# Performance work log

Hardware: AMD Instinct MI355X
Metric: run time of the kernel (lower is better)

## Reference

```python
import jax, jax.numpy as jnp
import numpy as np

DN = ('NCHW', 'OIHW', 'NCHW')

def conv(x, w, b=None, stride=(1, 1), pad=((0, 0), (0, 0))):
    y = jax.lax.conv_general_dilated(x, w, stride, pad, dimension_numbers=DN)
    return y if b is None else y + b[None, :, None, None]

def conv_t(x, w, b, stride, pad):
    # PyTorch ConvTranspose2d: weight (in, out, kH, kW), output (H-1)*s - 2p + k
    kH, kW = w.shape[2], w.shape[3]
    wt = jnp.flip(w, axis=(2, 3)).swapaxes(0, 1)  # -> (out, in, kH, kW)
    y = jax.lax.conv_general_dilated(
        x, wt, (1, 1),
        ((kH - 1 - pad[0], kH - 1 - pad[0]), (kW - 1 - pad[1], kW - 1 - pad[1])),
        lhs_dilation=stride, dimension_numbers=DN)
    return y + b[None, :, None, None]

def res_stack(x, rw1, rw2):
    # Residual: x + conv1x1(relu(conv3x3(relu(x)))), then final relu
    for i in range(rw1.shape[0]):
        h = conv(jax.nn.relu(x), rw1[i], None, (1, 1), ((1, 1), (1, 1)))
        h = conv(jax.nn.relu(h), rw2[i], None, (1, 1), ((0, 0), (0, 0)))
        x = x + h
    return jax.nn.relu(x)

def setup_inputs() -> dict:
    key = jax.random.key(0)
    ks = jax.random.split(key, 24)
    def w(i, shape, s=0.05):
        return jax.random.normal(ks[i], shape, jnp.float32) * s
    K, D = 512, 64
    inp = {
        'x': jax.random.normal(ks[0], (32, 2, 400, 600), jnp.float32),
        'enc_w1': w(1, (64, 2, 10, 11)), 'enc_b1': w(2, (64,)),
        'enc_w2': w(3, (128, 64, 12, 12), 0.02), 'enc_b2': w(4, (128,)),
        'enc_w3': w(5, (128, 128, 3, 3)), 'enc_b3': w(6, (128,)),
        'enc_res_w1': w(7, (2, 64, 128, 3, 3)), 'enc_res_w2': w(8, (2, 128, 64, 1, 1)),
        'pre_w': w(9, (64, 128, 1, 1)), 'pre_b': w(10, (64,)),
        'emb': jax.random.uniform(ks[11], (K, D), jnp.float32, -1.0 / K, 1.0 / K),
        'dec_w1': w(12, (128, 64, 3, 3)), 'dec_b1': w(13, (128,)),
        'dec_res_w1': w(14, (2, 64, 128, 3, 3)), 'dec_res_w2': w(15, (2, 128, 64, 1, 1)),
        'dec_tw1': w(16, (128, 64, 12, 12), 0.02), 'dec_tb1': w(17, (64,)),
        'dec_tw2': w(18, (64, 2, 10, 11)), 'dec_tb2': w(19, (2,)),
        'reset': 0,
    }
    return inp

def reference(x, enc_w1, enc_b1, enc_w2, enc_b2, enc_w3, enc_b3, enc_res_w1,
              enc_res_w2, pre_w, pre_b, emb, dec_w1, dec_b1, dec_res_w1,
              dec_res_w2, dec_tw1, dec_tb1, dec_tw2, dec_tb2, reset):
    commitment_cost = 0.25
    K = emb.shape[0]
    # Encoder
    h = jax.nn.relu(conv(x, enc_w1, enc_b1, (8, 9), ((1, 1), (1, 1))))
    h = jax.nn.relu(conv(h, enc_w2, enc_b2, (10, 10), ((1, 1), (1, 1))))
    h = conv(h, enc_w3, enc_b3, (1, 1), ((1, 1), (1, 1)))
    h = res_stack(h, enc_res_w1, enc_res_w2)
    z = conv(h, pre_w, pre_b)  # [B, D, H, W]
    # VectorQuantizer (eval mode)
    zin = z.transpose(0, 2, 3, 1)  # [B, H, W, D]
    B, H, W, D = zin.shape
    flat = zin.reshape(-1, D)
    dist = (jnp.sum(flat ** 2, axis=1, keepdims=True)
            + jnp.sum(emb ** 2, axis=1)
            - 2.0 * flat @ emb.T)  # [N, K]
    idx = jnp.argmin(dist, axis=1)  # [N]
    q = emb[idx].reshape(B, H, W, D)
    e_latent = jnp.mean((jax.lax.stop_gradient(q) - zin) ** 2)
    q_latent = jnp.mean((q - jax.lax.stop_gradient(zin)) ** 2)
    loss = q_latent + commitment_cost * e_latent
    q_st = zin + jax.lax.stop_gradient(q - zin)  # straight-through
    counts = jnp.zeros((K,), jnp.float32).at[idx].add(1.0)
    avg_probs = counts / flat.shape[0]
    perplexity = jnp.exp(-jnp.sum(avg_probs * jnp.log(avg_probs + 1e-10)))
    q_nchw = q_st.transpose(0, 3, 1, 2)
    # Decoder
    d = conv(q_nchw, dec_w1, dec_b1, (1, 1), ((1, 1), (1, 1)))
    d = res_stack(d, dec_res_w1, dec_res_w2)
    d = jax.nn.relu(conv_t(d, dec_tw1, dec_tb1, (10, 10), (1, 1)))
    recon = conv_t(d, dec_tw2, dec_tb2, (8, 9), (1, 1))
    return loss, recon, perplexity
```

## Files before the change

kernel.cpp:

```cpp
#include <hip/hip_runtime.h>
#include <math.h>


__global__ __launch_bounds__(256) void conv1_k(const float* __restrict__ x,
                                               const float* __restrict__ w,
                                               const float* __restrict__ b,
                                               float* __restrict__ y)
{
    __shared__ float xs[2 * 10 * 596];
    const int blk = blockIdx.x;
    const int n = blk / 50, oh = blk % 50;
    const int tid = threadIdx.x;
    const int ih0 = oh * 8 - 1;
    for (int i = tid; i < 2 * 10 * 596; i += 256) {
        int c = i / 5960, rem = i % 5960;
        int r = rem / 596, j = rem % 596;
        int ih = ih0 + r, iw = j - 1;
        float v = 0.f;
        if (ih >= 0 && ih < 400 && iw >= 0 && iw < 600)
            v = x[((n * 2 + c) * 400 + ih) * 600 + iw];
        xs[i] = v;
    }
    __syncthreads();
    for (int i = tid; i < 32 * 66; i += 256) {
        int oc = i / 66, ow = i % 66;
        int col = ow * 9;
        float a0 = 0.f, a1 = 0.f;
        for (int c = 0; c < 2; ++c) {
            const float* wp0 = w + ((oc)      * 2 + c) * 110;
            const float* wp1 = w + ((oc + 32) * 2 + c) * 110;
            const float* xp  = xs + c * 5960 + col;
            for (int kh = 0; kh < 10; ++kh) {
                #pragma unroll
                for (int kw = 0; kw < 11; ++kw) {
                    float xv = xp[kh * 596 + kw];
                    a0 += xv * wp0[kh * 11 + kw];
                    a1 += xv * wp1[kh * 11 + kw];
                }
            }
        }
        y[((n * 64 + oc)      * 50 + oh) * 66 + ow] = fmaxf(a0 + b[oc], 0.f);
        y[((n * 64 + oc + 32) * 50 + oh) * 66 + ow] = fmaxf(a1 + b[oc + 32], 0.f);
    }
}

__global__ __launch_bounds__(256) void repack_oihw_k(const float* __restrict__ w,
                                                     float* __restrict__ wt,
                                                     int OC, int IC, int KH, int KW)
{
    int i = blockIdx.x * 256 + threadIdx.x;
    int total = OC * IC * KH * KW;
    if (i >= total) return;
    int oc = i % OC; int t = i / OC;
    int kw = t % KW; int kh = (t / KW) % KH; int c = t / (KW * KH);
    wt[i] = w[((oc * IC + c) * KH + kh) * KW + kw];
}

__global__ __launch_bounds__(256) void repack_iohw_k(const float* __restrict__ w,
                                                     float* __restrict__ wt,
                                                     int IC, int OC, int KH, int KW)
{
    int i = blockIdx.x * 256 + threadIdx.x;
    int total = OC * IC * KH * KW;
    if (i >= total) return;
    int oc = i % OC; int t = i / OC;
    int kw = t % KW; int kh = (t / KW) % KH; int c = t / (KW * KH);
    wt[i] = w[((c * OC + oc) * KH + kh) * KW + kw];
}

__device__ __forceinline__ float fetch_oihw(const float* __restrict__ w, int j,
                                            int OC, int IC, int KH, int KW)
{
    int oc = j % OC; int t = j / OC;
    int kw = t % KW; int kh = (t / KW) % KH; int c = t / (KW * KH);
    return w[((oc * IC + c) * KH + kh) * KW + kw];
}

__global__ __launch_bounds__(256) void repack_small_k(
    const float* __restrict__ enc_w3, const float* __restrict__ er1,
    const float* __restrict__ er2, const float* __restrict__ pre_w,
    const float* __restrict__ dec_w1, const float* __restrict__ dr1,
    const float* __restrict__ dr2, float* __restrict__ dst)
{
    int i = blockIdx.x * 256 + threadIdx.x;
    if (i >= 557056) return;
    float v;
    if (i < 147456)       v = fetch_oihw(enc_w3,        i,          128, 128, 3, 3);
    else if (i < 221184)  v = fetch_oihw(er1,           i - 147456,  64, 128, 3, 3);
    else if (i < 294912)  v = fetch_oihw(er1 + 73728,   i - 221184,  64, 128, 3, 3);
    else if (i < 303104)  v = fetch_oihw(er2,           i - 294912, 128,  64, 1, 1);
    else if (i < 311296)  v = fetch_oihw(er2 + 8192,    i - 303104, 128,  64, 1, 1);
    else if (i < 319488)  v = fetch_oihw(pre_w,         i - 311296,  64, 128, 1, 1);
    else if (i < 393216)  v = fetch_oihw(dec_w1,        i - 319488, 128,  64, 3, 3);
    else if (i < 466944)  v = fetch_oihw(dr1,           i - 393216,  64, 128, 3, 3);
    else if (i < 540672)  v = fetch_oihw(dr1 + 73728,   i - 466944,  64, 128, 3, 3);
    else if (i < 548864)  v = fetch_oihw(dr2,           i - 540672, 128,  64, 1, 1);
    else                  v = fetch_oihw(dr2 + 8192,    i - 548864, 128,  64, 1, 1);
    dst[i] = v;
}

__global__ __launch_bounds__(512) void conv2_k2(const float* __restrict__ x,
                                                const float* __restrict__ wt,
                                                const float* __restrict__ b,
                                                float* __restrict__ y)
{
    __shared__ float xs[16 * 12 * 64];
    __shared__ float sred[4 * 128 * 6];
    const int tid = threadIdx.x;
    const int oc = tid & 127, sub = tid >> 7;
    const int n = blockIdx.x / 5, oh = blockIdx.x % 5;
    const int ih0 = oh * 10 - 1;
    float acc[6] = {0, 0, 0, 0, 0, 0};
    for (int cc = 0; cc < 4; ++cc) {
        __syncthreads();
        for (int i = tid; i < 12288; i += 512) {
            int col = i & 63; int t2 = i >> 6;
            int r = t2 % 12; int c = t2 / 12;
            int ih = ih0 + r, iw = col - 1;
            float v = 0.f;
            if (ih >= 0 && ih < 50 && iw >= 0 && iw < 66)
                v = x[((n * 64 + cc * 16 + c) * 50 + ih) * 66 + iw];
            xs[i] = v;
        }
        __syncthreads();
        for (int c = 0; c < 16; ++c) {
            for (int kh = sub * 3; kh < sub * 3 + 3; ++kh) {
                float xr[64];
                #pragma unroll
                for (int k = 0; k < 16; ++k)
                    *(float4*)&xr[4 * k] = *(const float4*)&xs[(c * 12 + kh) * 64 + 4 * k];
                const float* wp = wt + ((cc * 16 + c) * 144 + kh * 12) * 128 + oc;
                #pragma unroll
                for (int kw = 0; kw < 12; ++kw) {
                    float wv = wp[kw * 128];
                    #pragma unroll
                    for (int ow = 0; ow < 6; ++ow)
                        acc[ow] += xr[ow * 10 + kw] * wv;
                }
            }
        }
    }
    for (int j = 0; j < 6; ++j) sred[(sub * 128 + oc) * 6 + j] = acc[j];
    __syncthreads();
    if (sub == 0) {
        float bias = b[oc];
        #pragma unroll
        for (int j = 0; j < 6; ++j) {
            float v = acc[j] + sred[(128 + oc) * 6 + j] + sred[(256 + oc) * 6 + j]
                    + sred[(384 + oc) * 6 + j] + bias;
            y[((n * 128 + oc) * 5 + oh) * 6 + j] = fmaxf(v, 0.f);
        }
    }
}


template<int CIN, int COUT, bool RELU_IN>
__device__ __forceinline__ void conv3x3_stage(const float* __restrict__ src,
                                              const float* __restrict__ wg,
                                              const float* __restrict__ bias,
                                              float* __restrict__ dst,
                                              float* __restrict__ WS, int tid)
{
    constexpr int G  = 1024 / COUT;
    constexpr int NP = (30 + G - 1) / G;
    const int oc = tid % COUT;
    const int g  = tid / COUT;
    const int px0 = (30 * g) / G;
    const int np  = (30 * (g + 1)) / G - px0;
    float acc[NP];
    float bv = bias ? bias[oc] : 0.f;
    #pragma unroll
    for (int j = 0; j < NP; ++j) acc[j] = bv;
    for (int cc0 = 0; cc0 < CIN; cc0 += 16) {
        __syncthreads();
        const float* wsrc = wg + cc0 * 9 * COUT;
        for (int i = tid; i < 16 * 9 * COUT; i += 1024) WS[i] = wsrc[i];
        __syncthreads();
        for (int c = 0; c < 16; ++c) {
            const float* sc = src + (cc0 + c) * 30;
            const float* wc = WS + c * 9 * COUT + oc;
            #pragma unroll
            for (int kh = 0; kh < 3; ++kh) {
                #pragma unroll
                for (int kw = 0; kw < 3; ++kw) {
                    float wv = wc[(kh * 3 + kw) * COUT];
                    #pragma unroll
                    for (int j = 0; j < NP; ++j) {
                        if (j < np) {
                            int px = px0 + j;
                            int oh = px / 6, ow = px - oh * 6;
                            int ih = oh + kh - 1, iw = ow + kw - 1;
                            if ((unsigned)ih < 5u && (unsigned)iw < 6u) {
                                float xv = sc[ih * 6 + iw];
                                if (RELU_IN) xv = fmaxf(xv, 0.f);
                                acc[j] += xv * wv;
                            }
                        }
                    }
                }
            }
        }
    }
    #pragma unroll
    for (int j = 0; j < NP; ++j)
        if (j < np) dst[oc * 30 + px0 + j] = acc[j];
}

template<int CIN, int COUT, bool RELU_IN, bool ACCUM>
__device__ __forceinline__ void conv1x1_stage(const float* __restrict__ src,
                                              const float* __restrict__ wg,
                                              const float* __restrict__ bias,
                                              float* __restrict__ dst,
                                              float* __restrict__ WS, int tid)
{
    constexpr int G  = 1024 / COUT;
    constexpr int NP = (30 + G - 1) / G;
    const int oc = tid % COUT;
    const int g  = tid / COUT;
    const int px0 = (30 * g) / G;
    const int np  = (30 * (g + 1)) / G - px0;
    __syncthreads();
    for (int i = tid; i < CIN * COUT; i += 1024) WS[i] = wg[i];
    __syncthreads();
    float acc[NP];
    float bv = bias ? bias[oc] : 0.f;
    #pragma unroll
    for (int j = 0; j < NP; ++j) acc[j] = bv;
    for (int c = 0; c < CIN; ++c) {
        float wv = WS[c * COUT + oc];
        #pragma unroll
        for (int j = 0; j < NP; ++j) {
            if (j < np) {
                float xv = src[c * 30 + px0 + j];
                if (RELU_IN) xv = fmaxf(xv, 0.f);
                acc[j] += xv * wv;
            }
        }
    }
    #pragma unroll
    for (int j = 0; j < NP; ++j) {
        if (j < np) {
            if (ACCUM) dst[oc * 30 + px0 + j] += acc[j];
            else       dst[oc * 30 + px0 + j] = acc[j];
        }
    }
}

__global__ __launch_bounds__(1024) void chain_k(
    const float* __restrict__ h2, const float* __restrict__ wsm,
    const float* __restrict__ enc_b3, const float* __restrict__ pre_b,
    const float* __restrict__ emb, const float* __restrict__ dec_b1,
    float* __restrict__ xpad, float* __restrict__ counts,
    float* __restrict__ loss_sum)
{
    __shared__ float A[3840], B[3840], T[1920], Z[1920];
    __shared__ float WS[16 * 9 * 128];
    const int n = blockIdx.x;
    const int tid = threadIdx.x;
    for (int i = tid; i < 3840; i += 1024) A[i] = h2[n * 3840 + i];
    conv3x3_stage<128, 128, false>(A, wsm, enc_b3, B, WS, tid);
    conv3x3_stage<128, 64, true>(B, wsm + 147456, nullptr, T, WS, tid);
    conv1x1_stage<64, 128, true, true>(T, wsm + 294912, nullptr, B, WS, tid);
    conv3x3_stage<128, 64, true>(B, wsm + 221184, nullptr, T, WS, tid);
    conv1x1_stage<64, 128, true, true>(T, wsm + 303104, nullptr, B, WS, tid);
    conv1x1_stage<128, 64, true, false>(B, wsm + 311296, pre_b, Z, WS, tid);
    __syncthreads();
    const int lane = tid & 63, wid = tid >> 6;
    for (int px = wid; px < 30; px += 16) {
        float zr[64];
        #pragma unroll
        for (int d = 0; d < 64; ++d) zr[d] = Z[d * 30 + px];
        float best = 1e30f; int bestk = 0;
        for (int jk = 0; jk < 8; ++jk) {
            int k = lane + jk * 64;
            const float* ep = emb + k * 64;
            float dist = 0.f;
            #pragma unroll 8
            for (int d = 0; d < 64; ++d) { float df = ep[d] - zr[d]; dist += df * df; }
            if (dist < best) { best = dist; bestk = k; }
        }
        for (int off = 32; off; off >>= 1) {
            float ob = __shfl_down(best, off); int ok = __shfl_down(bestk, off);
            if (ob < best || (ob == best && ok < bestk)) { best = ob; bestk = ok; }
        }
        bestk = __shfl(bestk, 0);
        float ev = emb[bestk * 64 + lane];
        T[lane * 30 + px] = ev;
        float df = ev - Z[lane * 30 + px]; df *= df;
        for (int off = 32; off; off >>= 1) df += __shfl_down(df, off);
        if (lane == 0) { atomicAdd(loss_sum, df); atomicAdd(&counts[bestk], 1.f); }
    }
    __syncthreads();
    conv3x3_stage<64, 128, false>(T, wsm + 319488, dec_b1, A, WS, tid);
    conv3x3_stage<128, 64, true>(A, wsm + 393216, nullptr, T, WS, tid);
    conv1x1_stage<64, 128, true, true>(T, wsm + 540672, nullptr, A, WS, tid);
    conv3x3_stage<128, 64, true>(A, wsm + 466944, nullptr, T, WS, tid);
    conv1x1_stage<64, 128, true, true>(T, wsm + 548864, nullptr, A, WS, tid);
    __syncthreads();
    for (int i = tid; i < 7168; i += 1024) {
        int col = i & 7, r = (i >> 3) % 7, c = i / 56;
        float v = 0.f;
        if (r >= 1 && r <= 5 && col >= 1 && col <= 6)
            v = fmaxf(A[c * 30 + (r - 1) * 6 + col - 1], 0.f);
        xpad[n * 7168 + i] = v;
    }
}


template<bool TR, bool TS>
__device__ __forceinline__ void ct1_accum(const float* __restrict__ xs0,
                                          const float* __restrict__ xs1,
                                          const float* __restrict__ wt,
                                          int R, int S, int m0, int lane,
                                          float acc[6])
{
    #pragma unroll 2
    for (int c = 0; c < 128; ++c) {
        float x1[7], x0[7];
        #pragma unroll
        for (int k = 0; k < 7; ++k) x1[k] = xs1[c * 8 + m0 + k];
        if (TR) {
            #pragma unroll
            for (int k = 0; k < 7; ++k) x0[k] = xs0[c * 8 + m0 + k];
        }
        float wA = wt[(c * 144 + R * 12 + S) * 64 + lane];
        #pragma unroll
        for (int j = 0; j < 6; ++j) acc[j] += x1[j + 1] * wA;
        if (TS) {
            float wB = wt[(c * 144 + R * 12 + S + 10) * 64 + lane];
            #pragma unroll
            for (int j = 0; j < 6; ++j) acc[j] += x1[j] * wB;
        }
        if (TR) {
            float wC = wt[(c * 144 + (R + 10) * 12 + S) * 64 + lane];
            #pragma unroll
            for (int j = 0; j < 6; ++j) acc[j] += x0[j + 1] * wC;
            if (TS) {
                float wD = wt[(c * 144 + (R + 10) * 12 + S + 10) * 64 + lane];
                #pragma unroll
                for (int j = 0; j < 6; ++j) acc[j] += x0[j] * wD;
            }
        }
    }
}

__global__ __launch_bounds__(256) void convt1_k3(const float* __restrict__ xp,
                                                 const float* __restrict__ wt,
                                                 const float* __restrict__ b,
                                                 float* __restrict__ y)
{
    __shared__ float xs[2][128][8];
    const int bi = blockIdx.x;
    const int n = bi / 50, oh = bi % 50;
    const int q = (oh + 1) / 10, R = (oh + 1) % 10;
    const int tid = threadIdx.x;
    for (int i = tid; i < 2048; i += 256) {
        int col = i & 7, c = (i >> 3) & 127, r = i >> 10;
        ((float*)xs)[i] = xp[((n * 128 + c) * 7 + q + r) * 8 + col];
    }
    __syncthreads();
    const int lane = tid & 63, wv = tid >> 6;
    const float bias = b[lane];
    const float* xs0 = &xs[0][0][0];
    const float* xs1 = &xs[1][0][0];
    for (int si = 0; si < 3; ++si) {
        int S = wv + si * 4;
        if (S >= 10) break;
        int m0 = (S == 0) ? 1 : 0;
        float acc[6] = {0, 0, 0, 0, 0, 0};
        if (R < 2) {
            if (S < 2) ct1_accum<true, true>(xs0, xs1, wt, R, S, m0, lane, acc);
            else       ct1_accum<true, false>(xs0, xs1, wt, R, S, m0, lane, acc);
        } else {
            if (S < 2) ct1_accum<false, true>(xs0, xs1, wt, R, S, m0, lane, acc);
            else       ct1_accum<false, false>(xs0, xs1, wt, R, S, m0, lane, acc);
        }
        float* yp = y + ((n * 64 + lane) * 52 + oh + 1) * 62 + 10 * m0 + S;
        #pragma unroll
        for (int j = 0; j < 6; ++j) yp[10 * j] = fmaxf(acc[j] + bias, 0.f);
    }
}


template<bool TR, bool TS>
__device__ __forceinline__ void ct2_accum(const float* __restrict__ xs0,
                                          const float* __restrict__ xs1,
                                          const float* __restrict__ wt2,
                                          int R, int S, int m,
                                          float& a0, float& a1)
{
    #pragma unroll 4
    for (int c = 0; c < 64; ++c) {
        float x1a = xs1[c * 64 + m + 1];
        float2 wA = *(const float2*)&wt2[(c * 110 + R * 11 + S) * 2];
        a0 += x1a * wA.x; a1 += x1a * wA.y;
        if (TS) {
            float x1b = xs1[c * 64 + m];
            float2 wB = *(const float2*)&wt2[(c * 110 + R * 11 + S + 9) * 2];
            a0 += x1b * wB.x; a1 += x1b * wB.y;
        }
        if (TR) {
            float x0a = xs0[c * 64 + m + 1];
            float2 wC = *(const float2*)&wt2[(c * 110 + (R + 8) * 11 + S) * 2];
            a0 += x0a * wC.x; a1 += x0a * wC.y;
            if (TS) {
                float x0b = xs0[c * 64 + m];
                float2 wD = *(const float2*)&wt2[(c * 110 + (R + 8) * 11 + S + 9) * 2];
                a0 += x0b * wD.x; a1 += x0b * wD.y;
            }
        }
    }
}

__global__ __launch_bounds__(256) void convt2_k3(const float* __restrict__ xd,
                                                 const float* __restrict__ wt2,
                                                 const float* __restrict__ bb,
                                                 float* __restrict__ out)
{
    __shared__ float xs[2][64][64];
    const int bi = blockIdx.x;
    const int n = bi / 51, io = bi % 51;
    const int tid = threadIdx.x;
    for (int i = tid; i < 2 * 64 * 64; i += 256) {
        int col = i & 63, c = (i >> 6) & 63, r = i >> 12;
        float v = 0.f;
        if (col < 62) v = xd[((n * 64 + c) * 52 + io + r) * 62 + col];
        ((float*)xs)[i] = v;
    }
    __syncthreads();
    const float b0 = bb[0], b1 = bb[1];
    const int lane = tid & 63, wv = tid >> 6;
    if (lane < 60) {
        const float* xs0 = &xs[0][0][0];
        const float* xs1 = &xs[1][0][0];
        for (int pp = 0; pp < 18; ++pp) {
            int p = wv * 18 + pp;
            int R = p / 9, S = p % 9;
            int oh = 8 * io + R - 1;
            if (oh < 0 || oh >= 400) continue;
            int m = lane + ((S == 0) ? 1 : 0);
            float a0 = 0.f, a1 = 0.f;
            if (R < 2) {
                if (S < 2) ct2_accum<true, true>(xs0, xs1, wt2, R, S, m, a0, a1);
                else       ct2_accum<true, false>(xs0, xs1, wt2, R, S, m, a0, a1);
            } else {
                if (S < 2) ct2_accum<false, true>(xs0, xs1, wt2, R, S, m, a0, a1);
                else       ct2_accum<false, false>(xs0, xs1, wt2, R, S, m, a0, a1);
            }
            int ow = 9 * m + S - 1;
            float* yp = out + ((size_t)(n * 2) * 400 + oh) * 540 + ow;
            yp[0] = a0 + b0;
            yp[400 * 540] = a1 + b1;
        }
    }
}

__global__ __launch_bounds__(512) void fin_k(const float* __restrict__ counts,
                                             const float* __restrict__ loss_sum,
                                             float* __restrict__ out, int out_size)
{
    __shared__ float red[512];
    int t = threadIdx.x;
    float c = counts[t];
    float p = c * (1.0f / 960.0f);
    red[t] = p * logf(p + 1e-10f);
    __syncthreads();
    for (int s = 256; s > 0; s >>= 1) {
        if (t < s) red[t] += red[t + s];
        __syncthreads();
    }
    if (t == 0) {
        out[out_size - 1] = expf(-red[0]);
        out[0] = loss_sum[0] * 1.25f / 61440.0f;
    }
}

extern "C" void kernel_launch(void* const* d_in, const int* in_sizes, int n_in,
                              void* d_out, int out_size, void* d_ws, size_t ws_size,
                              hipStream_t stream)
{
    const float* x          = (const float*)d_in[0];
    const float* enc_w1     = (const float*)d_in[1];
    const float* enc_b1     = (const float*)d_in[2];
    const float* enc_w2     = (const float*)d_in[3];
    const float* enc_b2     = (const float*)d_in[4];
    const float* enc_w3     = (const float*)d_in[5];
    const float* enc_b3     = (const float*)d_in[6];
    const float* enc_res_w1 = (const float*)d_in[7];
    const float* enc_res_w2 = (const float*)d_in[8];
    const float* pre_w      = (const float*)d_in[9];
    const float* pre_b      = (const float*)d_in[10];
    const float* emb        = (const float*)d_in[11];
    const float* dec_w1     = (const float*)d_in[12];
    const float* dec_b1     = (const float*)d_in[13];
    const float* dec_res_w1 = (const float*)d_in[14];
    const float* dec_res_w2 = (const float*)d_in[15];
    const float* dec_tw1    = (const float*)d_in[16];
    const float* dec_tb1    = (const float*)d_in[17];
    const float* dec_tw2    = (const float*)d_in[18];
    const float* dec_tb2    = (const float*)d_in[19];

    float* ws  = (float*)d_ws;
    float* out = (float*)d_out;

    float* h1       = ws;
    float* dmid     = ws;
    float* h2       = ws + 6758400;
    float* counts   = ws + 6881280;
    float* loss_sum = ws + 6881792;
    float* wtA      = ws + 6881856;
    float* wt2      = ws + 8061504;
    float* xpad     = ws + 8075584;
    float* wsm      = ws + 8304960;

    hipMemsetAsync(counts, 0, 513 * sizeof(float), stream);

    repack_oihw_k<<<4608, 256, 0, stream>>>(enc_w2, wtA, 128, 64, 12, 12);
    conv1_k<<<1600, 256, 0, stream>>>(x, enc_w1, enc_b1, h1);
    conv2_k2<<<160, 512, 0, stream>>>(h1, wtA, enc_b2, h2);

    repack_small_k<<<2176, 256, 0, stream>>>(enc_w3, enc_res_w1, enc_res_w2, pre_w,
                                             dec_w1, dec_res_w1, dec_res_w2, wsm);
    chain_k<<<32, 1024, 0, stream>>>(h2, wsm, enc_b3, pre_b, emb, dec_b1,
                                     xpad, counts, loss_sum);

    repack_iohw_k<<<4608, 256, 0, stream>>>(dec_tw1, wtA, 128, 64, 12, 12);
    repack_iohw_k<<<55, 256, 0, stream>>>(dec_tw2, wt2, 64, 2, 10, 11);
    hipMemsetAsync(dmid, 0, (size_t)6602752 * sizeof(float), stream);
    convt1_k3<<<1600, 256, 0, stream>>>(xpad, wtA, dec_tb1, dmid);
    convt2_k3<<<1632, 256, 0, stream>>>(dmid, wt2, dec_tb2, out + 1);

    fin_k<<<1, 512, 0, stream>>>(counts, loss_sum, out, out_size);
}
```

Before: 2.249 ms.

## Split input channels across wave groups in chain kernel convs with shared-memory reduction

Rewrites the fused mid-network conv stages so each 64-thread group handles a slice of input channels for all 30 pixels, reading weights straight from global memory into registers. Partial sums are combined through two shared buffers with shared-memory atomics. This removes the staged weight copies into shared memory and the per-pixel bounds and index arithmetic. In exchange it needs large register arrays (up to 60 accumulators plus weights) at 1024 threads per block and adds atomic reduction traffic.

Result: faster. 2.177 ms (-3.2%).

```diff
diff --git a/kernel.cpp b/kernel.cpp
--- a/kernel.cpp
+++ b/kernel.cpp
@@ -154,96 +154,104 @@
 }
 
 
-template<int CIN, int COUT, bool RELU_IN>
-__device__ __forceinline__ void conv3x3_stage(const float* __restrict__ src,
-                                              const float* __restrict__ wg,
-                                              const float* __restrict__ bias,
-                                              float* __restrict__ dst,
-                                              float* __restrict__ WS, int tid)
-{
-    constexpr int G  = 1024 / COUT;
-    constexpr int NP = (30 + G - 1) / G;
-    const int oc = tid % COUT;
-    const int g  = tid / COUT;
-    const int px0 = (30 * g) / G;
-    const int np  = (30 * (g + 1)) / G - px0;
-    float acc[NP];
-    float bv = bias ? bias[oc] : 0.f;
+template<int CIN, int COUT, int KS, bool RELU_IN, bool ACCUM, bool HASBIAS>
+__device__ __forceinline__ void stagef(const float* __restrict__ src,
+                                       const float* __restrict__ wg,
+                                       const float* __restrict__ bias,
+                                       float* __restrict__ dst,
+                                       float* __restrict__ P,
+                                       float* __restrict__ Q,
+                                       int slot, int g)
+{
+    constexpr int OCPT = COUT / 64;
+    constexpr int CPT  = CIN / 16;
+    constexpr int NV   = 30 * OCPT;
+    constexpr int STR  = NV + 1;
+    float acc[OCPT][30];
     #pragma unroll
-    for (int j = 0; j < NP; ++j) acc[j] = bv;
-    for (int cc0 = 0; cc0 < CIN; cc0 += 16) {
-        __syncthreads();
-        const float* wsrc = wg + cc0 * 9 * COUT;
-        for (int i = tid; i < 16 * 9 * COUT; i += 1024) WS[i] = wsrc[i];
-        __syncthreads();
-        for (int c = 0; c < 16; ++c) {
-            const float* sc = src + (cc0 + c) * 30;
-            const float* wc = WS + c * 9 * COUT + oc;
-            #pragma unroll
-            for (int kh = 0; kh < 3; ++kh) {
-                #pragma unroll
-                for (int kw = 0; kw < 3; ++kw) {
-                    float wv = wc[(kh * 3 + kw) * COUT];
+    for (int o = 0; o < OCPT; ++o)
+        #pragma unroll
+        for (int j = 0; j < 30; ++j) acc[o][j] = 0.f;
+
+    const int c0 = g * CPT;
+    for (int cc = 0; cc < CPT; ++cc) {
+        const int c = c0 + cc;
+        const float* sc = src + c * 30;
+        if (KS == 3) {
+            const float* wp = wg + c * 9 * COUT + slot;
+            float w[OCPT][9];
+            #pragma unroll
+            for (int t = 0; t < 9; ++t)
+                #pragma unroll
+                for (int o = 0; o < OCPT; ++o) w[o][t] = wp[t * COUT + o * 64];
+            #pragma unroll
+            for (int rho = 0; rho < 5; ++rho) {
+                float xr[6];
+                #pragma unroll
+                for (int q2 = 0; q2 < 6; ++q2) {
+                    float xv = sc[rho * 6 + q2];
+                    xr[q2] = RELU_IN ? fmaxf(xv, 0.f) : xv;
+                }
+                #pragma unroll
+                for (int kh = 0; kh < 3; ++kh) {
+                    const int r = rho + 1 - kh;
+                    if (r < 0 || r > 4) continue;
                     #pragma unroll
-                    for (int j = 0; j < NP; ++j) {
-                        if (j < np) {
-                            int px = px0 + j;
-                            int oh = px / 6, ow = px - oh * 6;
-                            int ih = oh + kh - 1, iw = ow + kw - 1;
-                            if ((unsigned)ih < 5u && (unsigned)iw < 6u) {
-                                float xv = sc[ih * 6 + iw];
-                                if (RELU_IN) xv = fmaxf(xv, 0.f);
-                                acc[j] += xv * wv;
-                            }
+                    for (int kw = 0; kw < 3; ++kw) {
+                        #pragma unroll
+                        for (int pc = 0; pc < 6; ++pc) {
+                            const int gam = pc + kw - 1;
+                            if (gam < 0 || gam > 5) continue;
+                            #pragma unroll
+                            for (int o = 0; o < OCPT; ++o)
+                                acc[o][r * 6 + pc] += xr[gam] * w[o][kh * 3 + kw];
                         }
                     }
                 }
             }
-        }
-    }
-    #pragma unroll
-    for (int j = 0; j < NP; ++j)
-        if (j < np) dst[oc * 30 + px0 + j] = acc[j];
-}
-
-template<int CIN, int COUT, bool RELU_IN, bool ACCUM>
-__device__ __forceinline__ void conv1x1_stage(const float* __restrict__ src,
-                                              const float* __restrict__ wg,
-                                              const float* __restrict__ bias,
-                                              float* __restrict__ dst,
-                                              float* __restrict__ WS, int tid)
-{
-    constexpr int G  = 1024 / COUT;
-    constexpr int NP = (30 + G - 1) / G;
-    const int oc = tid % COUT;
-    const int g  = tid / COUT;
-    const int px0 = (30 * g) / G;
-    const int np  = (30 * (g + 1)) / G - px0;
-    __syncthreads();
-    for (int i = tid; i < CIN * COUT; i += 1024) WS[i] = wg[i];
-    __syncthreads();
-    float acc[NP];
-    float bv = bias ? bias[oc] : 0.f;
-    #pragma unroll
-    for (int j = 0; j < NP; ++j) acc[j] = bv;
-    for (int c = 0; c < CIN; ++c) {
-        float wv = WS[c * COUT + oc];
-        #pragma unroll
-        for (int j = 0; j < NP; ++j) {
-            if (j < np) {
-                float xv = src[c * 30 + px0 + j];
+        } else {
+            float w[OCPT];
+            #pragma unroll
+            for (int o = 0; o < OCPT; ++o) w[o] = wg[c * COUT + slot + o * 64];
+            #pragma unroll
+            for (int j = 0; j < 30; ++j) {
+                float xv = sc[j];
                 if (RELU_IN) xv = fmaxf(xv, 0.f);
-                acc[j] += xv * wv;
-            }
-        }
-    }
-    #pragma unroll
-    for (int j = 0; j < NP; ++j) {
-        if (j < np) {
-            if (ACCUM) dst[oc * 30 + px0 + j] += acc[j];
-            else       dst[oc * 30 + px0 + j] = acc[j];
-        }
-    }
+                #pragma unroll
+                for (int o = 0; o < OCPT; ++o) acc[o][j] += xv * w[o];
+            }
+        }
+    }
+    float* buf = (g < 8) ? Q : P;
+    if (g == 0 || g == 8) {
+        #pragma unroll
+        for (int o = 0; o < OCPT; ++o)
+            #pragma unroll
+            for (int j = 0; j < 30; ++j) buf[slot * STR + o * 30 + j] = acc[o][j];
+    }
+    __syncthreads();
+    if (g != 0 && g != 8) {
+        #pragma unroll
+        for (int o = 0; o < OCPT; ++o)
+            #pragma unroll
+            for (int j = 0; j < 30; ++j)
+                atomicAdd(&buf[slot * STR + o * 30 + j], acc[o][j]);
+    }
+    __syncthreads();
+    if (g == 0) {
+        #pragma unroll
+        for (int o = 0; o < OCPT; ++o) {
+            const int oc = slot + o * 64;
+            float bv = HASBIAS ? bias[oc] : 0.f;
+            #pragma unroll
+            for (int j = 0; j < 30; ++j) {
+                float v = Q[slot * STR + o * 30 + j] + P[slot * STR + o * 30 + j] + bv;
+                if (ACCUM) dst[oc * 30 + j] += v;
+                else       dst[oc * 30 + j] = v;
+            }
+        }
+    }
+    __syncthreads();
 }
 
 __global__ __launch_bounds__(1024) void chain_k(
@@ -254,25 +262,25 @@
     float* __restrict__ loss_sum)
 {
     __shared__ float A[3840], B[3840], T[1920], Z[1920];
-    __shared__ float WS[16 * 9 * 128];
+    __shared__ float P[64 * 61], Q[64 * 61];
     const int n = blockIdx.x;
     const int tid = threadIdx.x;
+    const int slot = tid & 63, g = tid >> 6;
     for (int i = tid; i < 3840; i += 1024) A[i] = h2[n * 3840 + i];
-    conv3x3_stage<128, 128, false>(A, wsm, enc_b3, B, WS, tid);
-    conv3x3_stage<128, 64, true>(B, wsm + 147456, nullptr, T, WS, tid);
-    conv1x1_stage<64, 128, true, true>(T, wsm + 294912, nullptr, B, WS, tid);
-    conv3x3_stage<128, 64, true>(B, wsm + 221184, nullptr, T, WS, tid);
-    conv1x1_stage<64, 128, true, true>(T, wsm + 303104, nullptr, B, WS, tid);
-    conv1x1_stage<128, 64, true, false>(B, wsm + 311296, pre_b, Z, WS, tid);
-    __syncthreads();
-    const int lane = tid & 63, wid = tid >> 6;
-    for (int px = wid; px < 30; px += 16) {
+    __syncthreads();
+    stagef<128, 128, 3, false, false, true>(A, wsm, enc_b3, B, P, Q, slot, g);
+    stagef<128, 64, 3, true, false, false>(B, wsm + 147456, nullptr, T, P, Q, slot, g);
+    stagef<64, 128, 1, true, true, false>(T, wsm + 294912, nullptr, B, P, Q, slot, g);
+    stagef<128, 64, 3, true, false, false>(B, wsm + 221184, nullptr, T, P, Q, slot, g);
+    stagef<64, 128, 1, true, true, false>(T, wsm + 303104, nullptr, B, P, Q, slot, g);
+    stagef<128, 64, 1, true, false, true>(B, wsm + 311296, pre_b, Z, P, Q, slot, g);
+    for (int px = g; px < 30; px += 16) {
         float zr[64];
         #pragma unroll
         for (int d = 0; d < 64; ++d) zr[d] = Z[d * 30 + px];
         float best = 1e30f; int bestk = 0;
         for (int jk = 0; jk < 8; ++jk) {
-            int k = lane + jk * 64;
+            int k = slot + jk * 64;
             const float* ep = emb + k * 64;
             float dist = 0.f;
             #pragma unroll 8
@@ -284,19 +292,18 @@
             if (ob < best || (ob == best && ok < bestk)) { best = ob; bestk = ok; }
         }
         bestk = __shfl(bestk, 0);
-        float ev = emb[bestk * 64 + lane];
-        T[lane * 30 + px] = ev;
-        float df = ev - Z[lane * 30 + px]; df *= df;
+        float ev = emb[bestk * 64 + slot];
+        T[slot * 30 + px] = ev;
+        float df = ev - Z[slot * 30 + px]; df *= df;
         for (int off = 32; off; off >>= 1) df += __shfl_down(df, off);
-        if (lane == 0) { atomicAdd(loss_sum, df); atomicAdd(&counts[bestk], 1.f); }
-    }
-    __syncthreads();
-    conv3x3_stage<64, 128, false>(T, wsm + 319488, dec_b1, A, WS, tid);
-    conv3x3_stage<128, 64, true>(A, wsm + 393216, nullptr, T, WS, tid);
-    conv1x1_stage<64, 128, true, true>(T, wsm + 540672, nullptr, A, WS, tid);
-    conv3x3_stage<128, 64, true>(A, wsm + 466944, nullptr, T, WS, tid);
-    conv1x1_stage<64, 128, true, true>(T, wsm + 548864, nullptr, A, WS, tid);
-    __syncthreads();
+        if (slot == 0) { atomicAdd(loss_sum, df); atomicAdd(&counts[bestk], 1.f); }
+    }
+    __syncthreads();
+    stagef<64, 128, 3, false, false, true>(T, wsm + 319488, dec_b1, A, P, Q, slot, g);
+    stagef<128, 64, 3, true, false, false>(A, wsm + 393216, nullptr, T, P, Q, slot, g);
+    stagef<64, 128, 1, true, true, false>(T, wsm + 540672, nullptr, A, P, Q, slot, g);
+    stagef<128, 64, 3, true, false, false>(A, wsm + 466944, nullptr, T, P, Q, slot, g);
+    stagef<64, 128, 1, true, true, false>(T, wsm + 548864, nullptr, A, P, Q, slot, g);
     for (int i = tid; i < 7168; i += 1024) {
         int col = i & 7, r = (i >> 3) % 7, c = i / 56;
         float v = 0.f;
```
